# Kernel tuning notes

Hardware: AMD Instinct MI355X
Metric: run time of the kernel (lower is better)

The kernel has to match this reference:

```python
import jax, jax.numpy as jnp
import numpy as np

EPS = 1e-6                                   # VN leaky-relu denominator eps
BN_SCALE = np.float32(1.0 / np.sqrt(1.0 + 1e-5))  # eval-mode BatchNorm with default stats
NEG = 0.2                                    # negative_slope


def vn_lin(x, w):
    # x: [n, c, 3, ...]; w: [c, o] -> [n, o, 3, ...]
    return jnp.einsum('nc...,co->no...', x, w)


def vn_act(p, d):
    # Vector-Neuron leaky ReLU: project p off the half-space defined by direction d.
    dot = jnp.sum(p * d, axis=2, keepdims=True)
    dsq = jnp.sum(d * d, axis=2, keepdims=True)
    corr = p - (dot / (dsq + EPS)) * d
    return NEG * p + (1.0 - NEG) * jnp.where(dot >= 0, p, corr)


def score_net(x, w_vn, wd_vn, w_h1, w_h2, b_h2, temp=1.0):
    # CorrelationNet: VNLinearLeakyReLU(3 -> 2*ks) -> norm -> 1x1 convs -> softmax
    p = vn_lin(x, w_vn) * BN_SCALE           # [N, 2ks, 3, K] (VNBatchNorm ~ scalar in eval)
    d = vn_lin(x, wd_vn)
    s = vn_act(p, d)
    s = jnp.linalg.norm(s, axis=2)           # [N, 2ks, K]
    s = jax.nn.relu(jnp.einsum('nck,co->nok', s, w_h1) * BN_SCALE)  # conv1d k=1, BN, relu
    s = jnp.einsum('nck,co->nok', s, w_h2) + b_h2[None, :, None]     # last conv with bias
    return jax.nn.softmax(s / temp, axis=1)  # [N, ks, K]


def setup_inputs() -> dict:
    key = jax.random.key(0)
    k = [jax.random.fold_in(key, i) for i in range(13)]
    N, N2, K, KS, OUT = 16000, 20000, 16, 8, 64
    half = OUT // 2
    return {
        'q_pts': jax.random.normal(k[0], (N, 3), jnp.float32),
        's_pts': jax.random.normal(k[1], (N2, 3), jnp.float32),
        's_feats': jax.random.normal(k[2], (N2, 1, 3), jnp.float32),
        'neighbor_indices': jax.random.randint(k[3], (N, K), 0, N2),
        'wb': jax.random.normal(k[4], (3, KS * half), jnp.float32) * np.float32(np.sqrt(2.0 / 3.0)),
        'w_vn': jax.random.normal(k[5], (3, 2 * KS), jnp.float32) * 0.5,
        'wd_vn': jax.random.normal(k[6], (3, 2 * KS), jnp.float32) * 0.5,
        'w_h1': jax.random.normal(k[7], (2 * KS, KS), jnp.float32) * 0.25,
        'w_h2': jax.random.normal(k[8], (KS, KS), jnp.float32) * 0.35,
        'b_h2': jnp.zeros((KS,), jnp.float32),
        'wd_relu': jax.random.normal(k[9], (half, half), jnp.float32) * 0.18,
        'w_un': jax.random.normal(k[10], (half, OUT), jnp.float32) * 0.18,
        'wd_un': jax.random.normal(k[11], (half, OUT), jnp.float32) * 0.18,
    }


def reference(q_pts, s_pts, s_feats, neighbor_indices, wb, w_vn, wd_vn,
              w_h1, w_h2, b_h2, wd_relu, w_un, wd_un):
    N, K = neighbor_indices.shape
    KS = w_h2.shape[1]
    # neighbor gather + centering: [N, K, 3] -> [N, 1, 3, K]
    pts = s_pts[neighbor_indices] - q_pts[:, None]
    pts = jnp.transpose(pts, (0, 2, 1))[:, None]
    centers = jnp.broadcast_to(jnp.mean(pts, axis=-1, keepdims=True), pts.shape)
    cross = jnp.cross(pts, centers, axis=2)
    local = jnp.concatenate([pts, centers, cross], axis=1)   # [N, 3, 3, K]
    scores = score_net(local, w_vn, wd_vn, w_h1, w_h2, b_h2)  # [N, KS, K]
    # kernel-point correlation conv
    pro = jnp.einsum('ncdk,cf->nfdk', local, wb)              # [N, KS*half, 3, K]
    pro = pro.reshape(N, KS, -1, 3, K)
    pro = jnp.sum(pro * scores[:, :, None, None, :], axis=1)  # [N, half, 3, K]
    nrm = jnp.linalg.norm(pro, axis=2, keepdims=True)
    normed = pro / jnp.maximum(nrm, 1e-12)                    # F.normalize(p=2, dim=2)
    feats = jnp.mean(normed, axis=-1)                         # [N, half, 3]
    feats = vn_act(feats, vn_lin(feats, wd_relu))             # VNLeakyReLU
    out = vn_act(vn_lin(feats, w_un) * BN_SCALE, vn_lin(feats, wd_un))  # VNLinearLeakyReLU
    return out                                                # [N, out_dim, 3]
```

## Files before the change

kernel.cpp:

```cpp
#include <hip/hip_runtime.h>
#include <math.h>

#define VN_EPS   1e-6f
#define NEG      0.2f
#define POS      0.8f

typedef float v2f __attribute__((ext_vector_type(2)));
typedef float v4f __attribute__((ext_vector_type(4)));

template <int CTRL>
__device__ __forceinline__ float dpp_add(float v) {
    int s = __builtin_amdgcn_update_dpp(0, __float_as_int(v), CTRL, 0xf, 0xf, true);
    return v + __int_as_float(s);
}
__device__ __forceinline__ float row16_allsum(float v) {
    v = dpp_add<0x128>(v);
    v = dpp_add<0x124>(v);
    v = dpp_add<0x122>(v);
    v = dpp_add<0x121>(v);
    return v;
}
__device__ __forceinline__ float row16_sum15(float v) {
    v = dpp_add<0x118>(v);
    v = dpp_add<0x114>(v);
    v = dpp_add<0x112>(v);
    v = dpp_add<0x111>(v);
    return v;
}
__device__ __forceinline__ float swz_xor16(float v) {
    return __int_as_float(__builtin_amdgcn_ds_swizzle(__float_as_int(v), 0x401F));
}

__global__ __launch_bounds__(128, 6) void areconv_kernel(
    const float* __restrict__ q_pts,
    const float* __restrict__ s_pts,
    const int*   __restrict__ nbr,
    const float* __restrict__ wb,
    const float* __restrict__ w_vn,
    const float* __restrict__ wd_vn,
    const float* __restrict__ w_h1,
    const float* __restrict__ w_h2,
    const float* __restrict__ b_h2,
    const float* __restrict__ wd_relu,
    const float* __restrict__ w_un,
    const float* __restrict__ wd_un,
    float* __restrict__ out,
    int N)
{
    const float BN_SCALE = 0.999994993f;

    __shared__ __align__(16) float featsA [4][3][36];
    __shared__ __align__(16) float feats2A[4][3][36];
    __shared__ __align__(16) float swb  [768];
    __shared__ __align__(16) float swvn [48];
    __shared__ __align__(16) float swdvn[48];
    __shared__ __align__(16) float swh1 [128];

    const int tid = threadIdx.x;
    if (tid < 48) { swvn[tid] = w_vn[tid]; swdvn[tid] = wd_vn[tid]; }
    swh1[tid] = w_h1[tid];
#pragma unroll
    for (int i = 0; i < 6; ++i) swb[tid + 128 * i] = wb[tid + 128 * i];
    __syncthreads();

    const int wv   = tid >> 6;
    const int lane = tid & 63;
    const int p    = lane >> 5;
    const int og   = (lane >> 4) & 1;
    const int k    = lane & 15;
    const int bp   = wv * 2 + p;
    int n = blockIdx.x * 4 + bp;
    n = (n < N) ? n : (N - 1);

    const float qx = q_pts[n * 3 + 0];
    const float qy = q_pts[n * 3 + 1];
    const float qz = q_pts[n * 3 + 2];
    const int   id = nbr[n * 16 + k];
    const float px = s_pts[id * 3 + 0] - qx;
    const float py = s_pts[id * 3 + 1] - qy;
    const float pz = s_pts[id * 3 + 2] - qz;

    const float cx = row16_allsum(px) * 0.0625f;
    const float cy = row16_allsum(py) * 0.0625f;
    const float cz = row16_allsum(pz) * 0.0625f;

    const float rx = py * cz - pz * cy;
    const float ry = pz * cx - px * cz;
    const float rz = px * cy - py * cx;

    const float L[3][3] = {{px, py, pz}, {cx, cy, cz}, {rx, ry, rz}};

    v2f t01 = {0.f, 0.f}, t23 = t01, t45 = t01, t67 = t01;
#pragma unroll 1
    for (int o8 = 0; o8 < 8; ++o8) {
        const int o = og * 8 + o8;
        const float wv0 = swvn[o],  wv1 = swvn[16 + o],  wv2 = swvn[32 + o];
        const float wd0 = swdvn[o], wd1 = swdvn[16 + o], wd2 = swdvn[32 + o];
        float pv[3], dv[3];
        float dot = 0.f, dsq = 0.f;
#pragma unroll
        for (int d = 0; d < 3; ++d) {
            const float pp = BN_SCALE * (L[0][d] * wv0 + L[1][d] * wv1 + L[2][d] * wv2);
            const float dd = L[0][d] * wd0 + L[1][d] * wd1 + L[2][d] * wd2;
            pv[d] = pp; dv[d] = dd;
            dot += pp * dd;
            dsq += dd * dd;
        }
        const float f = dot * __builtin_amdgcn_rcpf(dsq + VN_EPS);
        float acc = 0.f;
#pragma unroll
        for (int d = 0; d < 3; ++d) {
            const float corr = pv[d] - f * dv[d];
            const float sel  = (dot >= 0.f) ? pv[d] : corr;
            const float a    = NEG * pv[d] + POS * sel;
            acc += a * a;
        }
        const float s = __builtin_amdgcn_sqrtf(acc);
        t01 += s * (*(const v2f*)&swh1[o * 8 + 0]);
        t23 += s * (*(const v2f*)&swh1[o * 8 + 2]);
        t45 += s * (*(const v2f*)&swh1[o * 8 + 4]);
        t67 += s * (*(const v2f*)&swh1[o * 8 + 6]);
    }
    t01[0] += swz_xor16(t01[0]);  t01[1] += swz_xor16(t01[1]);
    t23[0] += swz_xor16(t23[0]);  t23[1] += swz_xor16(t23[1]);
    t45[0] += swz_xor16(t45[0]);  t45[1] += swz_xor16(t45[1]);
    t67[0] += swz_xor16(t67[0]);  t67[1] += swz_xor16(t67[1]);

    float tt[8];
    tt[0] = fmaxf(t01[0] * BN_SCALE, 0.f);  tt[1] = fmaxf(t01[1] * BN_SCALE, 0.f);
    tt[2] = fmaxf(t23[0] * BN_SCALE, 0.f);  tt[3] = fmaxf(t23[1] * BN_SCALE, 0.f);
    tt[4] = fmaxf(t45[0] * BN_SCALE, 0.f);  tt[5] = fmaxf(t45[1] * BN_SCALE, 0.f);
    tt[6] = fmaxf(t67[0] * BN_SCALE, 0.f);  tt[7] = fmaxf(t67[1] * BN_SCALE, 0.f);

    float sc[8];
    float mx = -1e30f;
#pragma unroll
    for (int op = 0; op < 4; ++op) {
        v2f u = *(const v2f*)&b_h2[2 * op];
#pragma unroll
        for (int c = 0; c < 8; ++c)
            u += tt[c] * (*(const v2f*)&w_h2[c * 8 + 2 * op]);
        sc[2 * op + 0] = u[0];
        sc[2 * op + 1] = u[1];
        mx = fmaxf(mx, fmaxf(u[0], u[1]));
    }
    float se = 0.f;
#pragma unroll
    for (int o = 0; o < 8; ++o) { sc[o] = __expf(sc[o] - mx); se += sc[o]; }
    const float inv_se = __builtin_amdgcn_rcpf(se);
#pragma unroll
    for (int o = 0; o < 8; ++o) sc[o] *= inv_se;

#pragma unroll 1
    for (int gi = 0; gi < 4; ++gi) {
        const int hb = og * 16 + gi * 4;
        v4f W0 = sc[0] * (*(const v4f*)&swb[0 * 256 + hb]);
        v4f W1 = sc[0] * (*(const v4f*)&swb[1 * 256 + hb]);
        v4f W2 = sc[0] * (*(const v4f*)&swb[2 * 256 + hb]);
#pragma unroll
        for (int s = 1; s < 8; ++s) {
            const float sv = sc[s];
            W0 += sv * (*(const v4f*)&swb[0 * 256 + s * 32 + hb]);
            W1 += sv * (*(const v4f*)&swb[1 * 256 + s * 32 + hb]);
            W2 += sv * (*(const v4f*)&swb[2 * 256 + s * 32 + hb]);
        }
        v4f V0 = L[0][0] * W0 + L[1][0] * W1 + L[2][0] * W2;
        v4f V1 = L[0][1] * W0 + L[1][1] * W1 + L[2][1] * W2;
        v4f V2 = L[0][2] * W0 + L[1][2] * W1 + L[2][2] * W2;
        const v4f vv = V0 * V0 + V1 * V1 + V2 * V2;
#pragma unroll
        for (int e = 0; e < 4; ++e) {
            const float inn = __builtin_amdgcn_rsqf(fmaxf(vv[e], 1e-24f)) * 0.0625f;
            V0[e] = row16_sum15(V0[e] * inn);
            V1[e] = row16_sum15(V1[e] * inn);
            V2[e] = row16_sum15(V2[e] * inn);
        }
        if (k == 15) {
            *(v4f*)&featsA[bp][0][hb] = V0;
            *(v4f*)&featsA[bp][1][hb] = V1;
            *(v4f*)&featsA[bp][2][hb] = V2;
        }
    }

    const int oo = og * 16 + k;

    {
        float D0 = 0.f, D1 = 0.f, D2 = 0.f;
#pragma unroll 1
        for (int grp = 0; grp < 8; ++grp) {
            const int hb = grp * 4;
            const v4f f0 = *(const v4f*)&featsA[bp][0][hb];
            const v4f f1 = *(const v4f*)&featsA[bp][1][hb];
            const v4f f2 = *(const v4f*)&featsA[bp][2][hb];
#pragma unroll
            for (int e = 0; e < 4; ++e) {
                const float w = wd_relu[(hb + e) * 32 + oo];
                D0 += f0[e] * w;
                D1 += f1[e] * w;
                D2 += f2[e] * w;
            }
        }
        const float p0 = featsA[bp][0][oo];
        const float p1 = featsA[bp][1][oo];
        const float p2 = featsA[bp][2][oo];
        const float dot = p0 * D0 + p1 * D1 + p2 * D2;
        const float dsq = D0 * D0 + D1 * D1 + D2 * D2;
        const float f   = dot * __builtin_amdgcn_rcpf(dsq + VN_EPS);
        const bool  pos = (dot >= 0.f);
        feats2A[bp][0][oo] = NEG * p0 + POS * (pos ? p0 : (p0 - f * D0));
        feats2A[bp][1][oo] = NEG * p1 + POS * (pos ? p1 : (p1 - f * D1));
        feats2A[bp][2][oo] = NEG * p2 + POS * (pos ? p2 : (p2 - f * D2));
    }

    {
        v2f AU0 = {0.f, 0.f}, AU1 = AU0, AU2 = AU0;
        v2f AV0 = AU0, AV1 = AU0, AV2 = AU0;
#pragma unroll 1
        for (int grp = 0; grp < 8; ++grp) {
            const int hb = grp * 4;
            const v4f f0 = *(const v4f*)&feats2A[bp][0][hb];
            const v4f f1 = *(const v4f*)&feats2A[bp][1][hb];
            const v4f f2 = *(const v4f*)&feats2A[bp][2][hb];
#pragma unroll
            for (int e = 0; e < 4; ++e) {
                const v2f wu = *(const v2f*)&w_un [(hb + e) * 64 + 2 * oo];
                const v2f wd = *(const v2f*)&wd_un[(hb + e) * 64 + 2 * oo];
                AU0 += f0[e] * wu; AU1 += f1[e] * wu; AU2 += f2[e] * wu;
                AV0 += f0[e] * wd; AV1 += f1[e] * wd; AV2 += f2[e] * wd;
            }
        }
        float O[6];
#pragma unroll
        for (int j = 0; j < 2; ++j) {
            const float u0 = AU0[j] * BN_SCALE;
            const float u1 = AU1[j] * BN_SCALE;
            const float u2 = AU2[j] * BN_SCALE;
            const float v0 = AV0[j], v1 = AV1[j], v2 = AV2[j];
            const float dot = u0 * v0 + u1 * v1 + u2 * v2;
            const float dsq = v0 * v0 + v1 * v1 + v2 * v2;
            const float f   = dot * __builtin_amdgcn_rcpf(dsq + VN_EPS);
            const bool  pos = (dot >= 0.f);
            O[3 * j + 0] = NEG * u0 + POS * (pos ? u0 : (u0 - f * v0));
            O[3 * j + 1] = NEG * u1 + POS * (pos ? u1 : (u1 - f * v1));
            O[3 * j + 2] = NEG * u2 + POS * (pos ? u2 : (u2 - f * v2));
        }
        float* dst = out + (long)n * 192 + 6 * oo;
        *(v2f*)(dst + 0) = *(const v2f*)&O[0];
        *(v2f*)(dst + 2) = *(const v2f*)&O[2];
        *(v2f*)(dst + 4) = *(const v2f*)&O[4];
    }
}

extern "C" void kernel_launch(void* const* d_in, const int* in_sizes, int n_in,
                              void* d_out, int out_size, void* d_ws, size_t ws_size,
                              hipStream_t stream) {
    const float* q_pts   = (const float*)d_in[0];
    const float* s_pts   = (const float*)d_in[1];
    const int*   nbr     = (const int*)  d_in[3];
    const float* wb      = (const float*)d_in[4];
    const float* w_vn    = (const float*)d_in[5];
    const float* w_h1    = (const float*)d_in[7];
    const float* wd_vn   = (const float*)d_in[6];
    const float* w_h2    = (const float*)d_in[8];
    const float* b_h2    = (const float*)d_in[9];
    const float* wd_relu = (const float*)d_in[10];
    const float* w_un    = (const float*)d_in[11];
    const float* wd_un   = (const float*)d_in[12];
    float* out = (float*)d_out;

    const int N = in_sizes[0] / 3;
    const int blocks = (N + 3) / 4;
    areconv_kernel<<<blocks, 128, 0, stream>>>(
        q_pts, s_pts, nbr, wb, w_vn, wd_vn, w_h1, w_h2, b_h2,
        wd_relu, w_un, wd_un, out, N);
}
```

Baseline: 129.2 us.

## Split fused kernel into correlation-fold and VN post-processing kernels

The single fused kernel is split in two. The first computes the scored, normalised and averaged features and writes them to the output buffer as scratch, working on 2-wide instead of 4-wide channel groups. The second kernel reads those features back, applies the VN leaky ReLU and the final VN linear leaky ReLU, and overwrites the output in place. The aim is to lower register and LDS pressure in the heavy kernel so more blocks fit per CU, and to run the light post stage at its own higher occupancy. The cost is a second launch plus an extra global write and read of about 12 MB of intermediate features.

New measurement: 124.9 us. -3.3%, faster.

```diff
diff --git a/kernel.cpp b/kernel.cpp
--- a/kernel.cpp
+++ b/kernel.cpp
@@ -31,7 +31,7 @@
     return __int_as_float(__builtin_amdgcn_ds_swizzle(__float_as_int(v), 0x401F));
 }
 
-__global__ __launch_bounds__(128, 6) void areconv_kernel(
+__global__ __launch_bounds__(128, 7) void areconv_fold(
     const float* __restrict__ q_pts,
     const float* __restrict__ s_pts,
     const int*   __restrict__ nbr,
@@ -41,16 +41,11 @@
     const float* __restrict__ w_h1,
     const float* __restrict__ w_h2,
     const float* __restrict__ b_h2,
-    const float* __restrict__ wd_relu,
-    const float* __restrict__ w_un,
-    const float* __restrict__ wd_un,
     float* __restrict__ out,
     int N)
 {
     const float BN_SCALE = 0.999994993f;
 
-    __shared__ __align__(16) float featsA [4][3][36];
-    __shared__ __align__(16) float feats2A[4][3][36];
     __shared__ __align__(16) float swb  [768];
     __shared__ __align__(16) float swvn [48];
     __shared__ __align__(16) float swdvn[48];
@@ -152,82 +147,100 @@
     for (int o = 0; o < 8; ++o) sc[o] *= inv_se;
 
 #pragma unroll 1
-    for (int gi = 0; gi < 4; ++gi) {
-        const int hb = og * 16 + gi * 4;
-        v4f W0 = sc[0] * (*(const v4f*)&swb[0 * 256 + hb]);
-        v4f W1 = sc[0] * (*(const v4f*)&swb[1 * 256 + hb]);
-        v4f W2 = sc[0] * (*(const v4f*)&swb[2 * 256 + hb]);
+    for (int gi = 0; gi < 8; ++gi) {
+        const int hb = og * 16 + gi * 2;
+        v2f W0 = sc[0] * (*(const v2f*)&swb[0 * 256 + hb]);
+        v2f W1 = sc[0] * (*(const v2f*)&swb[1 * 256 + hb]);
+        v2f W2 = sc[0] * (*(const v2f*)&swb[2 * 256 + hb]);
 #pragma unroll
         for (int s = 1; s < 8; ++s) {
             const float sv = sc[s];
-            W0 += sv * (*(const v4f*)&swb[0 * 256 + s * 32 + hb]);
-            W1 += sv * (*(const v4f*)&swb[1 * 256 + s * 32 + hb]);
-            W2 += sv * (*(const v4f*)&swb[2 * 256 + s * 32 + hb]);
-        }
-        v4f V0 = L[0][0] * W0 + L[1][0] * W1 + L[2][0] * W2;
-        v4f V1 = L[0][1] * W0 + L[1][1] * W1 + L[2][1] * W2;
-        v4f V2 = L[0][2] * W0 + L[1][2] * W1 + L[2][2] * W2;
-        const v4f vv = V0 * V0 + V1 * V1 + V2 * V2;
-#pragma unroll
-        for (int e = 0; e < 4; ++e) {
+            W0 += sv * (*(const v2f*)&swb[0 * 256 + s * 32 + hb]);
+            W1 += sv * (*(const v2f*)&swb[1 * 256 + s * 32 + hb]);
+            W2 += sv * (*(const v2f*)&swb[2 * 256 + s * 32 + hb]);
+        }
+        v2f V0 = L[0][0] * W0 + L[1][0] * W1 + L[2][0] * W2;
+        v2f V1 = L[0][1] * W0 + L[1][1] * W1 + L[2][1] * W2;
+        v2f V2 = L[0][2] * W0 + L[1][2] * W1 + L[2][2] * W2;
+        const v2f vv = V0 * V0 + V1 * V1 + V2 * V2;
+#pragma unroll
+        for (int e = 0; e < 2; ++e) {
             const float inn = __builtin_amdgcn_rsqf(fmaxf(vv[e], 1e-24f)) * 0.0625f;
             V0[e] = row16_sum15(V0[e] * inn);
             V1[e] = row16_sum15(V1[e] * inn);
             V2[e] = row16_sum15(V2[e] * inn);
         }
         if (k == 15) {
-            *(v4f*)&featsA[bp][0][hb] = V0;
-            *(v4f*)&featsA[bp][1][hb] = V1;
-            *(v4f*)&featsA[bp][2][hb] = V2;
-        }
-    }
-
-    const int oo = og * 16 + k;
+            float* dst = out + (long)n * 192;
+            *(v2f*)(dst +  0 + hb) = V0;
+            *(v2f*)(dst + 32 + hb) = V1;
+            *(v2f*)(dst + 64 + hb) = V2;
+        }
+    }
+}
+
+__global__ __launch_bounds__(256, 8) void areconv_post(
+    const float* __restrict__ wd_relu,
+    const float* __restrict__ w_un,
+    const float* __restrict__ wd_un,
+    float* __restrict__ out,
+    int N)
+{
+    const float BN_SCALE = 0.999994993f;
+
+    __shared__ float sf [8][96];
+    __shared__ float sf2[8][96];
+
+    const int tid  = threadIdx.x;
+    const int wv   = tid >> 6;
+    const int lane = tid & 63;
+    const int half = lane >> 5;
+    const int oo   = lane & 31;
+    const int bpi  = wv * 2 + half;
+
+    const int n0 = blockIdx.x * 8 + wv * 2;
+#pragma unroll
+    for (int i = lane; i < 192; i += 64) {
+        const int pt = (i >= 96) ? 1 : 0;
+        const int j  = i - 96 * pt;
+        int nn = n0 + pt;
+        nn = (nn < N) ? nn : (N - 1);
+        sf[wv * 2 + pt][j] = out[(long)nn * 192 + j];
+    }
+    int n = blockIdx.x * 8 + bpi;
+    n = (n < N) ? n : (N - 1);
 
     {
         float D0 = 0.f, D1 = 0.f, D2 = 0.f;
-#pragma unroll 1
-        for (int grp = 0; grp < 8; ++grp) {
-            const int hb = grp * 4;
-            const v4f f0 = *(const v4f*)&featsA[bp][0][hb];
-            const v4f f1 = *(const v4f*)&featsA[bp][1][hb];
-            const v4f f2 = *(const v4f*)&featsA[bp][2][hb];
-#pragma unroll
-            for (int e = 0; e < 4; ++e) {
-                const float w = wd_relu[(hb + e) * 32 + oo];
-                D0 += f0[e] * w;
-                D1 += f1[e] * w;
-                D2 += f2[e] * w;
-            }
-        }
-        const float p0 = featsA[bp][0][oo];
-        const float p1 = featsA[bp][1][oo];
-        const float p2 = featsA[bp][2][oo];
+        for (int h = 0; h < 32; ++h) {
+            const float w = wd_relu[h * 32 + oo];
+            D0 += sf[bpi][h]      * w;
+            D1 += sf[bpi][32 + h] * w;
+            D2 += sf[bpi][64 + h] * w;
+        }
+        const float p0 = sf[bpi][oo];
+        const float p1 = sf[bpi][32 + oo];
+        const float p2 = sf[bpi][64 + oo];
         const float dot = p0 * D0 + p1 * D1 + p2 * D2;
         const float dsq = D0 * D0 + D1 * D1 + D2 * D2;
         const float f   = dot * __builtin_amdgcn_rcpf(dsq + VN_EPS);
         const bool  pos = (dot >= 0.f);
-        feats2A[bp][0][oo] = NEG * p0 + POS * (pos ? p0 : (p0 - f * D0));
-        feats2A[bp][1][oo] = NEG * p1 + POS * (pos ? p1 : (p1 - f * D1));
-        feats2A[bp][2][oo] = NEG * p2 + POS * (pos ? p2 : (p2 - f * D2));
+        sf2[bpi][oo]      = NEG * p0 + POS * (pos ? p0 : (p0 - f * D0));
+        sf2[bpi][32 + oo] = NEG * p1 + POS * (pos ? p1 : (p1 - f * D1));
+        sf2[bpi][64 + oo] = NEG * p2 + POS * (pos ? p2 : (p2 - f * D2));
     }
 
     {
         v2f AU0 = {0.f, 0.f}, AU1 = AU0, AU2 = AU0;
         v2f AV0 = AU0, AV1 = AU0, AV2 = AU0;
-#pragma unroll 1
-        for (int grp = 0; grp < 8; ++grp) {
-            const int hb = grp * 4;
-            const v4f f0 = *(const v4f*)&feats2A[bp][0][hb];
-            const v4f f1 = *(const v4f*)&feats2A[bp][1][hb];
-            const v4f f2 = *(const v4f*)&feats2A[bp][2][hb];
-#pragma unroll
-            for (int e = 0; e < 4; ++e) {
-                const v2f wu = *(const v2f*)&w_un [(hb + e) * 64 + 2 * oo];
-                const v2f wd = *(const v2f*)&wd_un[(hb + e) * 64 + 2 * oo];
-                AU0 += f0[e] * wu; AU1 += f1[e] * wu; AU2 += f2[e] * wu;
-                AV0 += f0[e] * wd; AV1 += f1[e] * wd; AV2 += f2[e] * wd;
-            }
+        for (int h = 0; h < 32; ++h) {
+            const v2f wu = *(const v2f*)&w_un [h * 64 + 2 * oo];
+            const v2f wd = *(const v2f*)&wd_un[h * 64 + 2 * oo];
+            const float f0 = sf2[bpi][h];
+            const float f1 = sf2[bpi][32 + h];
+            const float f2 = sf2[bpi][64 + h];
+            AU0 += f0 * wu; AU1 += f1 * wu; AU2 += f2 * wu;
+            AV0 += f0 * wd; AV1 += f1 * wd; AV2 += f2 * wd;
         }
         float O[6];
 #pragma unroll
@@ -259,8 +272,8 @@
     const int*   nbr     = (const int*)  d_in[3];
     const float* wb      = (const float*)d_in[4];
     const float* w_vn    = (const float*)d_in[5];
+    const float* wd_vn   = (const float*)d_in[6];
     const float* w_h1    = (const float*)d_in[7];
-    const float* wd_vn   = (const float*)d_in[6];
     const float* w_h2    = (const float*)d_in[8];
     const float* b_h2    = (const float*)d_in[9];
     const float* wd_relu = (const float*)d_in[10];
@@ -269,8 +282,8 @@
     float* out = (float*)d_out;
 
     const int N = in_sizes[0] / 3;
-    const int blocks = (N + 3) / 4;
-    areconv_kernel<<<blocks, 128, 0, stream>>>(
-        q_pts, s_pts, nbr, wb, w_vn, wd_vn, w_h1, w_h2, b_h2,
+    areconv_fold<<<(N + 3) / 4, 128, 0, stream>>>(
+        q_pts, s_pts, nbr, wb, w_vn, wd_vn, w_h1, w_h2, b_h2, out, N);
+    areconv_post<<<(N + 7) / 8, 256, 0, stream>>>(
         wd_relu, w_un, wd_un, out, N);
 }
```

## Assign one wave per point with four output groups across 256-thread blocks

Applied to the files above, without the earlier changes.

Changes the work split from two points per wave (two output groups each) to one point per wave with four output groups of 16 lanes. Each lane now handles half as many score channels and kernel-correlation columns, and the tail VN stages compute one output per lane instead of two. Block size doubles to 256 so each block still covers four points. This raises thread-level parallelism and cuts per-thread serial work, at the cost of twice as many threads, duplicated neighbor-gather and score-net prologue work per lane, an extra cross-half shuffle reduction, and idle lanes in the VN leaky-ReLU stage.

Result: faster. 119.2 us (-7.8%).

```diff
diff --git a/kernel.cpp b/kernel.cpp
--- a/kernel.cpp
+++ b/kernel.cpp
@@ -30,8 +30,13 @@
 __device__ __forceinline__ float swz_xor16(float v) {
     return __int_as_float(__builtin_amdgcn_ds_swizzle(__float_as_int(v), 0x401F));
 }
-
-__global__ __launch_bounds__(128, 6) void areconv_kernel(
+__device__ __forceinline__ float og4_reduce(float v) {
+    v += swz_xor16(v);
+    v += __shfl_xor(v, 32, 64);
+    return v;
+}
+
+__global__ __launch_bounds__(256) void areconv_all(
     const float* __restrict__ q_pts,
     const float* __restrict__ s_pts,
     const int*   __restrict__ nbr,
@@ -49,27 +54,25 @@
 {
     const float BN_SCALE = 0.999994993f;
 
-    __shared__ __align__(16) float featsA [4][3][36];
-    __shared__ __align__(16) float feats2A[4][3][36];
     __shared__ __align__(16) float swb  [768];
     __shared__ __align__(16) float swvn [48];
     __shared__ __align__(16) float swdvn[48];
     __shared__ __align__(16) float swh1 [128];
+    __shared__ __align__(16) float sfeat [4][3][32];
+    __shared__ __align__(16) float sfeat2[4][3][32];
 
     const int tid = threadIdx.x;
-    if (tid < 48) { swvn[tid] = w_vn[tid]; swdvn[tid] = wd_vn[tid]; }
-    swh1[tid] = w_h1[tid];
-#pragma unroll
-    for (int i = 0; i < 6; ++i) swb[tid + 128 * i] = wb[tid + 128 * i];
+    if (tid < 48)  { swvn[tid] = w_vn[tid]; swdvn[tid] = wd_vn[tid]; }
+    if (tid < 128) swh1[tid] = w_h1[tid];
+#pragma unroll
+    for (int i = 0; i < 3; ++i) swb[tid + 256 * i] = wb[tid + 256 * i];
     __syncthreads();
 
     const int wv   = tid >> 6;
     const int lane = tid & 63;
-    const int p    = lane >> 5;
-    const int og   = (lane >> 4) & 1;
+    const int og   = lane >> 4;
     const int k    = lane & 15;
-    const int bp   = wv * 2 + p;
-    int n = blockIdx.x * 4 + bp;
+    int n = blockIdx.x * 4 + wv;
     n = (n < N) ? n : (N - 1);
 
     const float qx = q_pts[n * 3 + 0];
@@ -92,8 +95,8 @@
 
     v2f t01 = {0.f, 0.f}, t23 = t01, t45 = t01, t67 = t01;
 #pragma unroll 1
-    for (int o8 = 0; o8 < 8; ++o8) {
-        const int o = og * 8 + o8;
+    for (int o4 = 0; o4 < 4; ++o4) {
+        const int o = og * 4 + o4;
         const float wv0 = swvn[o],  wv1 = swvn[16 + o],  wv2 = swvn[32 + o];
         const float wd0 = swdvn[o], wd1 = swdvn[16 + o], wd2 = swdvn[32 + o];
         float pv[3], dv[3];
@@ -121,10 +124,10 @@
         t45 += s * (*(const v2f*)&swh1[o * 8 + 4]);
         t67 += s * (*(const v2f*)&swh1[o * 8 + 6]);
     }
-    t01[0] += swz_xor16(t01[0]);  t01[1] += swz_xor16(t01[1]);
-    t23[0] += swz_xor16(t23[0]);  t23[1] += swz_xor16(t23[1]);
-    t45[0] += swz_xor16(t45[0]);  t45[1] += swz_xor16(t45[1]);
-    t67[0] += swz_xor16(t67[0]);  t67[1] += swz_xor16(t67[1]);
+    t01[0] = og4_reduce(t01[0]);  t01[1] = og4_reduce(t01[1]);
+    t23[0] = og4_reduce(t23[0]);  t23[1] = og4_reduce(t23[1]);
+    t45[0] = og4_reduce(t45[0]);  t45[1] = og4_reduce(t45[1]);
+    t67[0] = og4_reduce(t67[0]);  t67[1] = og4_reduce(t67[1]);
 
     float tt[8];
     tt[0] = fmaxf(t01[0] * BN_SCALE, 0.f);  tt[1] = fmaxf(t01[1] * BN_SCALE, 0.f);
@@ -153,101 +156,95 @@
 
 #pragma unroll 1
     for (int gi = 0; gi < 4; ++gi) {
-        const int hb = og * 16 + gi * 4;
-        v4f W0 = sc[0] * (*(const v4f*)&swb[0 * 256 + hb]);
-        v4f W1 = sc[0] * (*(const v4f*)&swb[1 * 256 + hb]);
-        v4f W2 = sc[0] * (*(const v4f*)&swb[2 * 256 + hb]);
+        const int hb = og * 8 + gi * 2;
+        v2f W0 = sc[0] * (*(const v2f*)&swb[0 * 256 + hb]);
+        v2f W1 = sc[0] * (*(const v2f*)&swb[1 * 256 + hb]);
+        v2f W2 = sc[0] * (*(const v2f*)&swb[2 * 256 + hb]);
 #pragma unroll
         for (int s = 1; s < 8; ++s) {
             const float sv = sc[s];
-            W0 += sv * (*(const v4f*)&swb[0 * 256 + s * 32 + hb]);
-            W1 += sv * (*(const v4f*)&swb[1 * 256 + s * 32 + hb]);
-            W2 += sv * (*(const v4f*)&swb[2 * 256 + s * 32 + hb]);
-        }
-        v4f V0 = L[0][0] * W0 + L[1][0] * W1 + L[2][0] * W2;
-        v4f V1 = L[0][1] * W0 + L[1][1] * W1 + L[2][1] * W2;
-        v4f V2 = L[0][2] * W0 + L[1][2] * W1 + L[2][2] * W2;
-        const v4f vv = V0 * V0 + V1 * V1 + V2 * V2;
-#pragma unroll
-        for (int e = 0; e < 4; ++e) {
+            W0 += sv * (*(const v2f*)&swb[0 * 256 + s * 32 + hb]);
+            W1 += sv * (*(const v2f*)&swb[1 * 256 + s * 32 + hb]);
+            W2 += sv * (*(const v2f*)&swb[2 * 256 + s * 32 + hb]);
+        }
+        v2f V0 = L[0][0] * W0 + L[1][0] * W1 + L[2][0] * W2;
+        v2f V1 = L[0][1] * W0 + L[1][1] * W1 + L[2][1] * W2;
+        v2f V2 = L[0][2] * W0 + L[1][2] * W1 + L[2][2] * W2;
+        const v2f vv = V0 * V0 + V1 * V1 + V2 * V2;
+#pragma unroll
+        for (int e = 0; e < 2; ++e) {
             const float inn = __builtin_amdgcn_rsqf(fmaxf(vv[e], 1e-24f)) * 0.0625f;
             V0[e] = row16_sum15(V0[e] * inn);
             V1[e] = row16_sum15(V1[e] * inn);
             V2[e] = row16_sum15(V2[e] * inn);
         }
         if (k == 15) {
-            *(v4f*)&featsA[bp][0][hb] = V0;
-            *(v4f*)&featsA[bp][1][hb] = V1;
-            *(v4f*)&featsA[bp][2][hb] = V2;
-        }
-    }
-
-    const int oo = og * 16 + k;
-
+            *(v2f*)&sfeat[wv][0][hb] = V0;
+            *(v2f*)&sfeat[wv][1][hb] = V1;
+            *(v2f*)&sfeat[wv][2][hb] = V2;
+        }
+    }
+
+    const int oo = lane & 31;
     {
         float D0 = 0.f, D1 = 0.f, D2 = 0.f;
 #pragma unroll 1
-        for (int grp = 0; grp < 8; ++grp) {
-            const int hb = grp * 4;
-            const v4f f0 = *(const v4f*)&featsA[bp][0][hb];
-            const v4f f1 = *(const v4f*)&featsA[bp][1][hb];
-            const v4f f2 = *(const v4f*)&featsA[bp][2][hb];
+        for (int hq = 0; hq < 8; ++hq) {
+            const v4f f0 = *(const v4f*)&sfeat[wv][0][hq * 4];
+            const v4f f1 = *(const v4f*)&sfeat[wv][1][hq * 4];
+            const v4f f2 = *(const v4f*)&sfeat[wv][2][hq * 4];
 #pragma unroll
             for (int e = 0; e < 4; ++e) {
-                const float w = wd_relu[(hb + e) * 32 + oo];
+                const float w = wd_relu[(hq * 4 + e) * 32 + oo];
                 D0 += f0[e] * w;
                 D1 += f1[e] * w;
                 D2 += f2[e] * w;
             }
         }
-        const float p0 = featsA[bp][0][oo];
-        const float p1 = featsA[bp][1][oo];
-        const float p2 = featsA[bp][2][oo];
+        const float p0 = sfeat[wv][0][oo];
+        const float p1 = sfeat[wv][1][oo];
+        const float p2 = sfeat[wv][2][oo];
         const float dot = p0 * D0 + p1 * D1 + p2 * D2;
         const float dsq = D0 * D0 + D1 * D1 + D2 * D2;
         const float f   = dot * __builtin_amdgcn_rcpf(dsq + VN_EPS);
         const bool  pos = (dot >= 0.f);
-        feats2A[bp][0][oo] = NEG * p0 + POS * (pos ? p0 : (p0 - f * D0));
-        feats2A[bp][1][oo] = NEG * p1 + POS * (pos ? p1 : (p1 - f * D1));
-        feats2A[bp][2][oo] = NEG * p2 + POS * (pos ? p2 : (p2 - f * D2));
+        if (lane < 32) {
+            sfeat2[wv][0][oo] = NEG * p0 + POS * (pos ? p0 : (p0 - f * D0));
+            sfeat2[wv][1][oo] = NEG * p1 + POS * (pos ? p1 : (p1 - f * D1));
+            sfeat2[wv][2][oo] = NEG * p2 + POS * (pos ? p2 : (p2 - f * D2));
+        }
     }
 
     {
-        v2f AU0 = {0.f, 0.f}, AU1 = AU0, AU2 = AU0;
-        v2f AV0 = AU0, AV1 = AU0, AV2 = AU0;
-#pragma unroll 1
-        for (int grp = 0; grp < 8; ++grp) {
-            const int hb = grp * 4;
-            const v4f f0 = *(const v4f*)&feats2A[bp][0][hb];
-            const v4f f1 = *(const v4f*)&feats2A[bp][1][hb];
-            const v4f f2 = *(const v4f*)&feats2A[bp][2][hb];
+        float AU0 = 0.f, AU1 = 0.f, AU2 = 0.f;
+        float AV0 = 0.f, AV1 = 0.f, AV2 = 0.f;
+#pragma unroll 1
+        for (int hq = 0; hq < 8; ++hq) {
+            const v4f f0 = *(const v4f*)&sfeat2[wv][0][hq * 4];
+            const v4f f1 = *(const v4f*)&sfeat2[wv][1][hq * 4];
+            const v4f f2 = *(const v4f*)&sfeat2[wv][2][hq * 4];
 #pragma unroll
             for (int e = 0; e < 4; ++e) {
-                const v2f wu = *(const v2f*)&w_un [(hb + e) * 64 + 2 * oo];
-                const v2f wd = *(const v2f*)&wd_un[(hb + e) * 64 + 2 * oo];
+                const float wu = w_un [(hq * 4 + e) * 64 + lane];
+                const float wd = wd_un[(hq * 4 + e) * 64 + lane];
                 AU0 += f0[e] * wu; AU1 += f1[e] * wu; AU2 += f2[e] * wu;
                 AV0 += f0[e] * wd; AV1 += f1[e] * wd; AV2 += f2[e] * wd;
             }
         }
-        float O[6];
-#pragma unroll
-        for (int j = 0; j < 2; ++j) {
-            const float u0 = AU0[j] * BN_SCALE;
-            const float u1 = AU1[j] * BN_SCALE;
-            const float u2 = AU2[j] * BN_SCALE;
-            const float v0 = AV0[j], v1 = AV1[j], v2 = AV2[j];
-            const float dot = u0 * v0 + u1 * v1 + u2 * v2;
-            const float dsq = v0 * v0 + v1 * v1 + v2 * v2;
-            const float f   = dot * __builtin_amdgcn_rcpf(dsq + VN_EPS);
-            const bool  pos = (dot >= 0.f);
-            O[3 * j + 0] = NEG * u0 + POS * (pos ? u0 : (u0 - f * v0));
-            O[3 * j + 1] = NEG * u1 + POS * (pos ? u1 : (u1 - f * v1));
-            O[3 * j + 2] = NEG * u2 + POS * (pos ? u2 : (u2 - f * v2));
-        }
-        float* dst = out + (long)n * 192 + 6 * oo;
-        *(v2f*)(dst + 0) = *(const v2f*)&O[0];
-        *(v2f*)(dst + 2) = *(const v2f*)&O[2];
-        *(v2f*)(dst + 4) = *(const v2f*)&O[4];
+        const float u0 = AU0 * BN_SCALE;
+        const float u1 = AU1 * BN_SCALE;
+        const float u2 = AU2 * BN_SCALE;
+        const float dot = u0 * AV0 + u1 * AV1 + u2 * AV2;
+        const float dsq = AV0 * AV0 + AV1 * AV1 + AV2 * AV2;
+        const float f   = dot * __builtin_amdgcn_rcpf(dsq + VN_EPS);
+        const bool  pos = (dot >= 0.f);
+        const float O0 = NEG * u0 + POS * (pos ? u0 : (u0 - f * AV0));
+        const float O1 = NEG * u1 + POS * (pos ? u1 : (u1 - f * AV1));
+        const float O2 = NEG * u2 + POS * (pos ? u2 : (u2 - f * AV2));
+        float* dst = out + (long)n * 192 + 3 * lane;
+        dst[0] = O0;
+        dst[1] = O1;
+        dst[2] = O2;
     }
 }
 
@@ -259,8 +256,8 @@
     const int*   nbr     = (const int*)  d_in[3];
     const float* wb      = (const float*)d_in[4];
     const float* w_vn    = (const float*)d_in[5];
+    const float* wd_vn   = (const float*)d_in[6];
     const float* w_h1    = (const float*)d_in[7];
-    const float* wd_vn   = (const float*)d_in[6];
     const float* w_h2    = (const float*)d_in[8];
     const float* b_h2    = (const float*)d_in[9];
     const float* wd_relu = (const float*)d_in[10];
@@ -270,7 +267,7 @@
 
     const int N = in_sizes[0] / 3;
     const int blocks = (N + 3) / 4;
-    areconv_kernel<<<blocks, 128, 0, stream>>>(
+    areconv_all<<<blocks, 256, 0, stream>>>(
         q_pts, s_pts, nbr, wb, w_vn, wd_vn, w_h1, w_h2, b_h2,
         wd_relu, w_un, wd_un, out, N);
 }
```
